# Performance work log

Measured on AMD Instinct MI355X. Metric: run time of the kernel, lower is better.

The kernel has to match this reference:

```python
import jax, jax.numpy as jnp
import numpy as np
from jax import lax

PATCH = 9
DILATION = 1
EPS = 1e-6


def _l2norm(x):
    # L2-normalize over channel dim (dim=1), eps added to sum of squares before sqrt
    norm = jnp.sqrt(jnp.sum(x * x, axis=1, keepdims=True) + EPS)
    return x / norm


def setup_inputs() -> dict:
    key = jax.random.key(0)
    k1, k2 = jax.random.split(key)
    feature1 = jax.random.normal(k1, (4, 64, 64, 64), dtype=jnp.float32)
    feature2 = jax.random.normal(k2, (4, 64, 64, 64), dtype=jnp.float32)
    return {"feature1": feature1, "feature2": feature2}


def _correlation(f1, f2, patch, dilation):
    # SpatialCorrelationSampler with ks=1, stride=1, pad=0:
    # corr[b, pi, pj, y, x] = sum_c f1[b,c,y,x] * f2[b,c,y+dy,x+dx]
    # dy = (pi - patch//2)*dilation, dx = (pj - patch//2)*dilation; OOB = 0.
    b, c, h, w = f1.shape
    half = (patch // 2) * dilation
    f2p = jnp.pad(f2, ((0, 0), (0, 0), (half, half), (half, half)))
    d = jnp.arange(patch, dtype=jnp.int32) * dilation  # offsets into padded map
    offs = jnp.stack(jnp.meshgrid(d, d, indexing="ij"), axis=-1).reshape(-1, 2)  # [P^2, 2]

    def one_disp(off):
        f2s = lax.dynamic_slice(f2p, (0, 0, off[0], off[1]), (b, c, h, w))
        return jnp.sum(f1 * f2s, axis=1)  # [b, h, w]

    corr = lax.map(one_disp, offs)  # [P^2, b, h, w] (sequential -> low peak memory)
    return jnp.transpose(corr, (1, 0, 2, 3))  # [b, P^2, h, w]


def reference(feature1, feature2):
    f1 = _l2norm(feature1)
    f2 = _l2norm(feature2)
    b, c, h, w = f1.shape
    corr = _correlation(f1, f2, PATCH, DILATION)  # [b, P^2, h, w]
    corr = corr.reshape(b, PATCH * PATCH, h * w)
    return jax.nn.relu(corr)
```

## Files before the change

kernel.cpp:

```cpp
#include <hip/hip_runtime.h>

#define BB 4
#define CC 64
#define C2 32
#define HH 64
#define WW 64
#define PATCH 9
#define HALF 4
#define P2 81
#define HW 4096
#define IMG (CC * HW)

typedef _Float16 v2h __attribute__((ext_vector_type(2)));

static __device__ __forceinline__ unsigned pk(float a, float b) {
    v2h h = {(_Float16)a, (_Float16)b};
    return __builtin_bit_cast(unsigned, h);
}

__global__ __launch_bounds__(64) void corr_kernel(const float* __restrict__ f1,
                                                  const float* __restrict__ f2,
                                                  float* __restrict__ out) {
    __shared__ unsigned sB[C2 * 72];
    __shared__ float sS2[64];

    const int x   = threadIdx.x;
    const int bid = blockIdx.x;
    const int xcd = bid & 7;
    const int s   = bid >> 3;
    const int b   = s / 72;
    const int r   = s - b * 72;
    const int yo  = r / 9;
    const int dy  = r - yo * 9;
    const int y   = xcd * 8 + yo;
    const int y2  = y + dy - HALF;

    float* ob = out + b * (P2 * HW) + y * WW + x;

    if ((unsigned)y2 >= HH) {
#pragma unroll
        for (int dx = 0; dx < PATCH; ++dx)
            ob[(dy * PATCH + dx) * HW] = 0.f;
        return;
    }

    const float* f1r = f1 + b * IMG + y * WW + x;
    unsigned a[C2];
    float ssq1 = 0.f;
#pragma unroll
    for (int c2 = 0; c2 < C2; ++c2) {
        float u0 = f1r[(2 * c2) * HW];
        float u1 = f1r[(2 * c2 + 1) * HW];
        ssq1 = fmaf(u0, u0, fmaf(u1, u1, ssq1));
        a[c2] = pk(u0, u1);
    }

    const float* f2r = f2 + b * IMG + y2 * WW;
#pragma unroll
    for (int it = 0; it < 8; ++it) {
        int item = x + it * 64;
        int c2 = item >> 4, k = item & 15;
        const float* p = f2r + 4 * k;
        float4 va = *(const float4*)(p + (2 * c2) * HW);
        float4 vb = *(const float4*)(p + (2 * c2 + 1) * HW);
        uint4 u = {pk(va.x, vb.x), pk(va.y, vb.y), pk(va.z, vb.z), pk(va.w, vb.w)};
        *(uint4*)&sB[c2 * 72 + 4 + 4 * k] = u;
    }
#pragma unroll
    for (int it = 0; it < 4; ++it) {
        int j = x + it * 64;
        int c2 = j >> 3, e = j & 7;
        sB[c2 * 72 + (e < 4 ? e : 64 + e)] = 0u;
    }
    __syncthreads();

    float acc[PATCH];
#pragma unroll
    for (int i = 0; i < PATCH; ++i) acc[i] = 0.f;
    float ssq2 = 0.f;
#pragma unroll
    for (int c2 = 0; c2 < C2; ++c2) {
        v2h a2 = __builtin_bit_cast(v2h, a[c2]);
        const unsigned* br = &sB[c2 * 72 + x];
#pragma unroll
        for (int dx = 0; dx < PATCH; ++dx)
            acc[dx] = __builtin_amdgcn_fdot2(a2, __builtin_bit_cast(v2h, br[dx]),
                                             acc[dx], false);
        v2h c4 = __builtin_bit_cast(v2h, br[4]);
        ssq2 = __builtin_amdgcn_fdot2(c4, c4, ssq2, false);
    }
    sS2[x] = rsqrtf(ssq2 + 1e-6f);
    __syncthreads();

    const float s1 = rsqrtf(ssq1 + 1e-6f);
#pragma unroll
    for (int dx = 0; dx < PATCH; ++dx) {
        int col = x + dx - HALF;
        col = min(max(col, 0), WW - 1);
        ob[(dy * PATCH + dx) * HW] = fmaxf(acc[dx] * s1 * sS2[col], 0.f);
    }
}

extern "C" void kernel_launch(void* const* d_in, const int* in_sizes, int n_in,
                              void* d_out, int out_size, void* d_ws, size_t ws_size,
                              hipStream_t stream) {
    const float* f1 = (const float*)d_in[0];
    const float* f2 = (const float*)d_in[1];
    float* out = (float*)d_out;
    (void)d_ws; (void)ws_size;

    corr_kernel<<<BB * HH * PATCH, 64, 0, stream>>>(f1, f2, out);
}
```

Baseline: 66.04 us.

## Split displacement columns across three wavefronts per block and use pkrtz conversion

Each block now runs three wavefronts, and each wavefront computes three of the nine horizontal displacements for a row, where before one wave did all nine. The f2 row staging into shared memory is shared across the 192 threads, and one wave computes the f2 norms from shared memory. Float-to-half packing now uses the hardware pkrtz instruction, and the f1 norm is computed from the rounded half values. Each wave still loads the full f1 column, so f1 global reads are tripled, and rounding toward zero changes precision slightly.

Result: slower. 72.56 us (+9.9%).

```diff
diff --git a/kernel.cpp b/kernel.cpp
--- a/kernel.cpp
+++ b/kernel.cpp
@@ -12,19 +12,22 @@
 #define IMG (CC * HW)
 
 typedef _Float16 v2h __attribute__((ext_vector_type(2)));
+typedef __fp16 v2fp __attribute__((ext_vector_type(2)));
 
-static __device__ __forceinline__ unsigned pk(float a, float b) {
-    v2h h = {(_Float16)a, (_Float16)b};
+static __device__ __forceinline__ unsigned pkrtz(float a, float b) {
+    v2fp h = __builtin_amdgcn_cvt_pkrtz(a, b);
     return __builtin_bit_cast(unsigned, h);
 }
 
-__global__ __launch_bounds__(64) void corr_kernel(const float* __restrict__ f1,
-                                                  const float* __restrict__ f2,
-                                                  float* __restrict__ out) {
+__global__ __launch_bounds__(192) void corr_kernel(const float* __restrict__ f1,
+                                                   const float* __restrict__ f2,
+                                                   float* __restrict__ out) {
     __shared__ unsigned sB[C2 * 72];
     __shared__ float sS2[64];
 
-    const int x   = threadIdx.x;
+    const int tid = threadIdx.x;
+    const int x   = tid & 63;
+    const int w   = tid >> 6;
     const int bid = blockIdx.x;
     const int xcd = bid & 7;
     const int s   = bid >> 3;
@@ -39,9 +42,24 @@
 
     if ((unsigned)y2 >= HH) {
 #pragma unroll
-        for (int dx = 0; dx < PATCH; ++dx)
-            ob[(dy * PATCH + dx) * HW] = 0.f;
+        for (int j = 0; j < 3; ++j)
+            ob[(dy * PATCH + 3 * w + j) * HW] = 0.f;
         return;
+    }
+
+    const float* f2r = f2 + b * IMG + y2 * WW;
+    for (int item = tid; item < 512; item += 192) {
+        int c2 = item >> 4, k = item & 15;
+        const float* p = f2r + 4 * k;
+        float4 va = *(const float4*)(p + (2 * c2) * HW);
+        float4 vb = *(const float4*)(p + (2 * c2 + 1) * HW);
+        uint4 u = {pkrtz(va.x, vb.x), pkrtz(va.y, vb.y),
+                   pkrtz(va.z, vb.z), pkrtz(va.w, vb.w)};
+        *(uint4*)&sB[c2 * 72 + 4 + 4 * k] = u;
+    }
+    for (int j = tid; j < 256; j += 192) {
+        int c2 = j >> 3, e = j & 7;
+        sB[c2 * 72 + (e < 4 ? e : 64 + e)] = 0u;
     }
 
     const float* f1r = f1 + b * IMG + y * WW + x;
@@ -51,53 +69,42 @@
     for (int c2 = 0; c2 < C2; ++c2) {
         float u0 = f1r[(2 * c2) * HW];
         float u1 = f1r[(2 * c2 + 1) * HW];
-        ssq1 = fmaf(u0, u0, fmaf(u1, u1, ssq1));
-        a[c2] = pk(u0, u1);
-    }
-
-    const float* f2r = f2 + b * IMG + y2 * WW;
-#pragma unroll
-    for (int it = 0; it < 8; ++it) {
-        int item = x + it * 64;
-        int c2 = item >> 4, k = item & 15;
-        const float* p = f2r + 4 * k;
-        float4 va = *(const float4*)(p + (2 * c2) * HW);
-        float4 vb = *(const float4*)(p + (2 * c2 + 1) * HW);
-        uint4 u = {pk(va.x, vb.x), pk(va.y, vb.y), pk(va.z, vb.z), pk(va.w, vb.w)};
-        *(uint4*)&sB[c2 * 72 + 4 + 4 * k] = u;
-    }
-#pragma unroll
-    for (int it = 0; it < 4; ++it) {
-        int j = x + it * 64;
-        int c2 = j >> 3, e = j & 7;
-        sB[c2 * 72 + (e < 4 ? e : 64 + e)] = 0u;
+        a[c2] = pkrtz(u0, u1);
+        v2h a2 = __builtin_bit_cast(v2h, a[c2]);
+        ssq1 = __builtin_amdgcn_fdot2(a2, a2, ssq1, false);
     }
     __syncthreads();
 
-    float acc[PATCH];
+    if (w == 0) {
+        float ss = 0.f;
 #pragma unroll
-    for (int i = 0; i < PATCH; ++i) acc[i] = 0.f;
-    float ssq2 = 0.f;
+        for (int c2 = 0; c2 < C2; ++c2) {
+            v2h v = __builtin_bit_cast(v2h, sB[c2 * 72 + 4 + x]);
+            ss = __builtin_amdgcn_fdot2(v, v, ss, false);
+        }
+        sS2[x] = rsqrtf(ss + 1e-6f);
+    }
+
+    float acc0 = 0.f, acc1 = 0.f, acc2 = 0.f;
+    const int boff = x + 3 * w;
 #pragma unroll
     for (int c2 = 0; c2 < C2; ++c2) {
         v2h a2 = __builtin_bit_cast(v2h, a[c2]);
-        const unsigned* br = &sB[c2 * 72 + x];
-#pragma unroll
-        for (int dx = 0; dx < PATCH; ++dx)
-            acc[dx] = __builtin_amdgcn_fdot2(a2, __builtin_bit_cast(v2h, br[dx]),
-                                             acc[dx], false);
-        v2h c4 = __builtin_bit_cast(v2h, br[4]);
-        ssq2 = __builtin_amdgcn_fdot2(c4, c4, ssq2, false);
+        const unsigned* br = &sB[c2 * 72 + boff];
+        acc0 = __builtin_amdgcn_fdot2(a2, __builtin_bit_cast(v2h, br[0]), acc0, false);
+        acc1 = __builtin_amdgcn_fdot2(a2, __builtin_bit_cast(v2h, br[1]), acc1, false);
+        acc2 = __builtin_amdgcn_fdot2(a2, __builtin_bit_cast(v2h, br[2]), acc2, false);
     }
-    sS2[x] = rsqrtf(ssq2 + 1e-6f);
     __syncthreads();
 
     const float s1 = rsqrtf(ssq1 + 1e-6f);
+    float accs[3] = {acc0, acc1, acc2};
 #pragma unroll
-    for (int dx = 0; dx < PATCH; ++dx) {
+    for (int j = 0; j < 3; ++j) {
+        int dx = 3 * w + j;
         int col = x + dx - HALF;
         col = min(max(col, 0), WW - 1);
-        ob[(dy * PATCH + dx) * HW] = fmaxf(acc[dx] * s1 * sS2[col], 0.f);
+        ob[(dy * PATCH + dx) * HW] = fmaxf(accs[j] * s1 * sS2[col], 0.f);
     }
 }
 
@@ -109,5 +116,5 @@
     float* out = (float*)d_out;
     (void)d_ws; (void)ws_size;
 
-    corr_kernel<<<BB * HH * PATCH, 64, 0, stream>>>(f1, f2, out);
+    corr_kernel<<<BB * HH * PATCH, 192, 0, stream>>>(f1, f2, out);
 }
```

## Share each staged f2 row across two adjacent output rows per block

Applied to the files above, without the earlier changes.

Each block now handles a pair of output rows, y0 and y0+1, against one f2 row. The staged f2 row in shared memory and its norm are reused by both rows, which cuts the grid from 2304 to 1280 blocks and reduces redundant f2 loading and packing. The f1 norm is now computed from fp16-packed values with fdot2, and conversion uses the packed round-toward-zero instruction. In exchange there are more registers per thread and slightly lower precision in the norms.

After: 69.92 us. 5.9% more time.

```diff
diff --git a/kernel.cpp b/kernel.cpp
--- a/kernel.cpp
+++ b/kernel.cpp
@@ -12,10 +12,15 @@
 #define IMG (CC * HW)
 
 typedef _Float16 v2h __attribute__((ext_vector_type(2)));
+typedef __fp16 v2fp __attribute__((ext_vector_type(2)));
 
-static __device__ __forceinline__ unsigned pk(float a, float b) {
-    v2h h = {(_Float16)a, (_Float16)b};
+static __device__ __forceinline__ unsigned pkrtz(float a, float b) {
+    v2fp h = __builtin_amdgcn_cvt_pkrtz(a, b);
     return __builtin_bit_cast(unsigned, h);
+}
+static __device__ __forceinline__ float fdot2u(unsigned a, unsigned b, float acc) {
+    return __builtin_amdgcn_fdot2(__builtin_bit_cast(v2h, a),
+                                  __builtin_bit_cast(v2h, b), acc, false);
 }
 
 __global__ __launch_bounds__(64) void corr_kernel(const float* __restrict__ f1,
@@ -28,31 +33,27 @@
     const int bid = blockIdx.x;
     const int xcd = bid & 7;
     const int s   = bid >> 3;
-    const int b   = s / 72;
-    const int r   = s - b * 72;
-    const int yo  = r / 9;
-    const int dy  = r - yo * 9;
-    const int y   = xcd * 8 + yo;
-    const int y2  = y + dy - HALF;
+    const int b   = s / 40;
+    const int r   = s - b * 40;
+    const int yp  = r / 10;
+    const int d   = r - yp * 10;
+    const int y0  = xcd * 8 + yp * 2;
+    const int y2  = y0 + d - HALF;
 
-    float* ob = out + b * (P2 * HW) + y * WW + x;
+    const bool has0 = (d <= 8);
+    const bool has1 = (d >= 1);
+
+    float* ob0 = out + b * (P2 * HW) + y0 * WW + x;
+    float* ob1 = ob0 + WW;
 
     if ((unsigned)y2 >= HH) {
+        if (has0)
 #pragma unroll
-        for (int dx = 0; dx < PATCH; ++dx)
-            ob[(dy * PATCH + dx) * HW] = 0.f;
+            for (int dx = 0; dx < PATCH; ++dx) ob0[(d * PATCH + dx) * HW] = 0.f;
+        if (has1)
+#pragma unroll
+            for (int dx = 0; dx < PATCH; ++dx) ob1[((d - 1) * PATCH + dx) * HW] = 0.f;
         return;
-    }
-
-    const float* f1r = f1 + b * IMG + y * WW + x;
-    unsigned a[C2];
-    float ssq1 = 0.f;
-#pragma unroll
-    for (int c2 = 0; c2 < C2; ++c2) {
-        float u0 = f1r[(2 * c2) * HW];
-        float u1 = f1r[(2 * c2 + 1) * HW];
-        ssq1 = fmaf(u0, u0, fmaf(u1, u1, ssq1));
-        a[c2] = pk(u0, u1);
     }
 
     const float* f2r = f2 + b * IMG + y2 * WW;
@@ -63,7 +64,8 @@
         const float* p = f2r + 4 * k;
         float4 va = *(const float4*)(p + (2 * c2) * HW);
         float4 vb = *(const float4*)(p + (2 * c2 + 1) * HW);
-        uint4 u = {pk(va.x, vb.x), pk(va.y, vb.y), pk(va.z, vb.z), pk(va.w, vb.w)};
+        uint4 u = {pkrtz(va.x, vb.x), pkrtz(va.y, vb.y),
+                   pkrtz(va.z, vb.z), pkrtz(va.w, vb.w)};
         *(uint4*)&sB[c2 * 72 + 4 + 4 * k] = u;
     }
 #pragma unroll
@@ -72,32 +74,51 @@
         int c2 = j >> 3, e = j & 7;
         sB[c2 * 72 + (e < 4 ? e : 64 + e)] = 0u;
     }
+
+    const float* f1r0 = f1 + b * IMG + y0 * WW + x;
+    unsigned a0[C2], a1[C2];
+    float ssq1a = 0.f, ssq1b = 0.f;
+#pragma unroll
+    for (int c2 = 0; c2 < C2; ++c2) {
+        float u0 = f1r0[(2 * c2) * HW];
+        float u1 = f1r0[(2 * c2 + 1) * HW];
+        a0[c2] = pkrtz(u0, u1);
+        ssq1a = fdot2u(a0[c2], a0[c2], ssq1a);
+        float w0 = f1r0[(2 * c2) * HW + WW];
+        float w1 = f1r0[(2 * c2 + 1) * HW + WW];
+        a1[c2] = pkrtz(w0, w1);
+        ssq1b = fdot2u(a1[c2], a1[c2], ssq1b);
+    }
     __syncthreads();
 
-    float acc[PATCH];
+    float acc0[PATCH], acc1[PATCH];
 #pragma unroll
-    for (int i = 0; i < PATCH; ++i) acc[i] = 0.f;
+    for (int i = 0; i < PATCH; ++i) { acc0[i] = 0.f; acc1[i] = 0.f; }
     float ssq2 = 0.f;
 #pragma unroll
     for (int c2 = 0; c2 < C2; ++c2) {
-        v2h a2 = __builtin_bit_cast(v2h, a[c2]);
         const unsigned* br = &sB[c2 * 72 + x];
+        unsigned p0 = a0[c2], p1 = a1[c2];
 #pragma unroll
-        for (int dx = 0; dx < PATCH; ++dx)
-            acc[dx] = __builtin_amdgcn_fdot2(a2, __builtin_bit_cast(v2h, br[dx]),
-                                             acc[dx], false);
-        v2h c4 = __builtin_bit_cast(v2h, br[4]);
-        ssq2 = __builtin_amdgcn_fdot2(c4, c4, ssq2, false);
+        for (int dx = 0; dx < PATCH; ++dx) {
+            unsigned bv = br[dx];
+            acc0[dx] = fdot2u(p0, bv, acc0[dx]);
+            acc1[dx] = fdot2u(p1, bv, acc1[dx]);
+        }
+        ssq2 = fdot2u(br[4], br[4], ssq2);
     }
     sS2[x] = rsqrtf(ssq2 + 1e-6f);
     __syncthreads();
 
-    const float s1 = rsqrtf(ssq1 + 1e-6f);
+    const float s1a = rsqrtf(ssq1a + 1e-6f);
+    const float s1b = rsqrtf(ssq1b + 1e-6f);
 #pragma unroll
     for (int dx = 0; dx < PATCH; ++dx) {
         int col = x + dx - HALF;
         col = min(max(col, 0), WW - 1);
-        ob[(dy * PATCH + dx) * HW] = fmaxf(acc[dx] * s1 * sS2[col], 0.f);
+        float s2 = sS2[col];
+        if (has0) ob0[(d * PATCH + dx) * HW] = fmaxf(acc0[dx] * s1a * s2, 0.f);
+        if (has1) ob1[((d - 1) * PATCH + dx) * HW] = fmaxf(acc1[dx] * s1b * s2, 0.f);
     }
 }
 
@@ -109,5 +130,5 @@
     float* out = (float*)d_out;
     (void)d_ws; (void)ws_size;
 
-    corr_kernel<<<BB * HH * PATCH, 64, 0, stream>>>(f1, f2, out);
+    corr_kernel<<<BB * (HH / 2) * (PATCH + 1), 64, 0, stream>>>(f1, f2, out);
 }
```
